# Optimization experiments

Measured on AMD Instinct MI355X. Metric: run time of the kernel, lower is better.

## Reference

```python
import jax, jax.numpy as jnp
import numpy as np

L = 16384          # leaves of complete binary tree
D = 256            # word_dim == tree_input_dim == output_dim
V = 50257          # num_words
NL = 5             # num_labels


def setup_inputs() -> dict:
    key = jax.random.key(0)
    ks = jax.random.split(key, 8)
    s = 0.05
    return {
        "tokens": jax.random.randint(ks[0], (L,), 0, V),
        "emb": jax.random.normal(ks[1], (V, D), jnp.float32) * s,      # word_embedding.weight
        "Wx": jax.random.normal(ks[2], (D, 5 * D), jnp.float32) * s,   # input->gates (leaf only)
        "Ul": jax.random.normal(ks[3], (D, 5 * D), jnp.float32) * s,   # left-child h -> gates
        "Ur": jax.random.normal(ks[4], (D, 5 * D), jnp.float32) * s,   # right-child h -> gates
        "b": jnp.zeros((5 * D,), jnp.float32),
        "Wp": jax.random.normal(ks[5], (D, NL), jnp.float32) * s,      # pred_layer
        "bp": jnp.zeros((NL,), jnp.float32),
    }


def _cell(pre, c_l, c_r):
    # Binary TreeLSTM cell: gates [i, f_l, f_r, o, u]
    i, fl, fr, o, u = jnp.split(pre, 5, axis=-1)
    c = jax.nn.sigmoid(i) * jnp.tanh(u) + jax.nn.sigmoid(fl) * c_l + jax.nn.sigmoid(fr) * c_r
    h = jax.nn.sigmoid(o) * jnp.tanh(c)
    return h, c


def reference(tokens, emb, Wx, Ul, Ur, b, Wp, bp):
    # dropout layers are identity at inference (no-op here)
    x = emb[tokens]                                  # [L, D] seq_output == word embeddings (leaf_rnn=False)
    # leaf nodes: l/r child states are zeros, inputs = seq_out[idx]
    h, c = _cell(x @ Wx + b, 0.0, 0.0)               # [L, D]
    hs = [h]
    # internal nodes level by level (complete binary tree): inputs=None -> no Wx term
    while h.shape[0] > 1:
        hl, hr = h[0::2], h[1::2]
        cl, cr = c[0::2], c[1::2]
        h, c = _cell(hl @ Ul + hr @ Ur + b, cl, cr)
        hs.append(h)
    hidden = jnp.concatenate(hs, axis=0)             # [2L-1, D] all node hidden states
    return hidden @ Wp + bp                          # single_h_pred logits [2L-1, NL]
```

## Files before the change

### kernel.cpp

```cpp
#include <hip/hip_runtime.h>
#include <hip/hip_bf16.h>
#include <math.h>
#include <stdint.h>


typedef __attribute__((ext_vector_type(8))) short     bf16x8;
typedef __attribute__((ext_vector_type(4))) float     f32x4;
typedef __attribute__((ext_vector_type(8))) unsigned short u16x8;

#define NGATE 5

__device__ __forceinline__ uint16_t f2bf(float f) {
    uint32_t u = __builtin_bit_cast(uint32_t, f);
    u = (u + 0x7fffu + ((u >> 16) & 1u)) >> 16;
    return (uint16_t)u;
}
__device__ __forceinline__ float bf2f(uint16_t h) {
    uint32_t u = ((uint32_t)h) << 16;
    return __builtin_bit_cast(float, u);
}
__device__ __forceinline__ float sigf(float x) { return 1.0f / (1.0f + __expf(-x)); }
__device__ __forceinline__ float tanhfast(float x) {
    float e = __expf(2.0f * x);
    return (e - 1.0f) / (e + 1.0f);
}

__device__ __forceinline__ void gld_lds16(const void* g, void* l) {
    __builtin_amdgcn_global_load_lds(
        (const __attribute__((address_space(1))) void*)g,
        (__attribute__((address_space(3))) void*)l,
        16, 0, 0);
}

__global__ __launch_bounds__(256) void pack_w_kernel(
    const float* __restrict__ W0, const float* __restrict__ W1, int KT,
    uint16_t* __restrict__ dhi, uint16_t* __restrict__ dlo)
{
    int gid = blockIdx.x * 256 + threadIdx.x;
    int total = 80 * KT * 64;
    if (gid >= total) return;
    int lane = gid & 63;
    int n  = ((gid >> 6) / KT) * 16 + (lane & 15);
    int kt = (gid >> 6) % KT;
    int k0 = kt * 32 + (lane >> 4) * 8;
    u16x8 vh, vl;
    #pragma unroll
    for (int j = 0; j < 8; ++j) {
        int k = k0 + j;
        const float* src = (k < 256) ? (W0 + (size_t)k * 1280)
                                     : (W1 + (size_t)(k - 256) * 1280);
        float v = src[n];
        uint16_t h = f2bf(v);
        vh[j] = h;
        vl[j] = f2bf(v - bf2f(h));
    }
    *(u16x8*)(dhi + (size_t)gid * 8) = vh;
    *(u16x8*)(dlo + (size_t)gid * 8) = vl;
}

template<int BM, int KT, int JT, bool LVL0>
__global__ __launch_bounds__(256) void lvl_gemm(
    const uint16_t* __restrict__ Ahi, const uint16_t* __restrict__ Alo,
    const int* __restrict__ tokens, const float* __restrict__ emb,
    const uint16_t* __restrict__ Bhi, const uint16_t* __restrict__ Blo,
    const float* __restrict__ b,
    const float* __restrict__ c_prev,
    uint16_t* __restrict__ h_hi_out, uint16_t* __restrict__ h_lo_out,
    float* __restrict__ c_out, int n)
{
    constexpr int K   = KT * 32;
    constexpr int MT  = BM / 64;
    constexpr int ACH = BM / 16;
    constexpr int NC  = NGATE * JT * 2;

    __shared__ __align__(16) uint16_t lA0[2][BM * 32];
    __shared__ __align__(16) uint16_t lA1[2][BM * 32];
    __shared__ __align__(16) uint16_t lB0[NC * 512];
    __shared__ __align__(16) uint16_t lB1[NC * 512];

    const int tid  = threadIdx.x;
    const int wave = tid >> 6;
    const int lane = tid & 63;
    const int quad = lane >> 4;
    const int l15  = lane & 15;
    const int r0   = blockIdx.x * BM;
    const int jn   = blockIdx.y;

    f32x4 acc[MT][JT][NGATE] = {};

    const int row0 = tid >> 1;
    const int kh   = tid & 1;
    const float* esrc = nullptr;
    if constexpr (LVL0) {
        int tok = tokens[r0 + row0];
        esrc = emb + (size_t)tok * 256 + kh * 16;
    }

    auto stageB = [&](uint16_t* dB, int kt) {
        for (int c = wave; c < NC; c += 4) {
            int hl = c & 1, gj = c >> 1;
            const uint16_t* src = hl ? Blo : Bhi;
            int nt = (gj / JT) * 16 + jn * JT + (gj % JT);
            gld_lds16(src + ((size_t)(nt * KT + kt) * 64 + lane) * 8,
                      dB + c * 512);
        }
    };
    auto stageA = [&](uint16_t* dA0, uint16_t* dA1, int kt) {
        for (int c = wave; c < 2 * ACH; c += 4) {
            int mat = (c >= ACH) ? 1 : 0;
            int ci  = mat ? (c - ACH) : c;
            const uint16_t* src = mat ? Alo : Ahi;
            uint16_t* dst = (mat ? dA1 : dA0) + ci * 512;
            int row = r0 + ci * 16 + l15;
            row = min(row, n - 1);
            gld_lds16(src + (size_t)row * K + kt * 32 + quad * 8, dst);
        }
    };
    auto stage0 = [&](uint16_t* dA0, uint16_t* dA1, uint16_t* dB, int kt) {
        stageB(dB, kt);
        const float* s = esrc + kt * 32;
        float v[16];
        #pragma unroll
        for (int q = 0; q < 4; ++q) {
            float4 f = *(const float4*)(s + 4 * q);
            v[4*q+0] = f.x; v[4*q+1] = f.y; v[4*q+2] = f.z; v[4*q+3] = f.w;
        }
        u16x8 h0, h1, l0, l1;
        #pragma unroll
        for (int j = 0; j < 8; ++j) {
            uint16_t h = f2bf(v[j]);     h0[j] = h; l0[j] = f2bf(v[j]     - bf2f(h));
            uint16_t g2 = f2bf(v[j+8]);  h1[j] = g2; l1[j] = f2bf(v[j+8] - bf2f(g2));
        }
        int o = (row0 >> 4) * 512 + kh * 256 + (row0 & 15) * 8;
        *(u16x8*)(dA0 + o)       = h0;
        *(u16x8*)(dA0 + o + 128) = h1;
        *(u16x8*)(dA1 + o)       = l0;
        *(u16x8*)(dA1 + o + 128) = l1;
    };
    auto compute = [&](const uint16_t* A0, const uint16_t* A1, const uint16_t* Bx) {
        bf16x8 ah[MT], al[MT];
        #pragma unroll
        for (int mt = 0; mt < MT; ++mt) {
            int ci = wave * MT + mt;
            ah[mt] = *(const bf16x8*)(A0 + ci * 512 + lane * 8);
            al[mt] = *(const bf16x8*)(A1 + ci * 512 + lane * 8);
        }
        #pragma unroll
        for (int g = 0; g < NGATE; ++g) {
            #pragma unroll
            for (int js = 0; js < JT; ++js) {
                const uint16_t* bp = Bx + (g * JT + js) * 1024;
                bf16x8 bh = *(const bf16x8*)(bp + lane * 8);
                bf16x8 bl = *(const bf16x8*)(bp + 512 + lane * 8);
                #pragma unroll
                for (int mt = 0; mt < MT; ++mt) {
                    acc[mt][js][g] = __builtin_amdgcn_mfma_f32_16x16x32_bf16(ah[mt], bh, acc[mt][js][g], 0, 0, 0);
                    acc[mt][js][g] = __builtin_amdgcn_mfma_f32_16x16x32_bf16(al[mt], bh, acc[mt][js][g], 0, 0, 0);
                    acc[mt][js][g] = __builtin_amdgcn_mfma_f32_16x16x32_bf16(ah[mt], bl, acc[mt][js][g], 0, 0, 0);
                }
            }
        }
    };

    if constexpr (LVL0) stage0(lA0[0], lA0[1], lB0, 0);
    else { stageA(lA0[0], lA0[1], 0); stageB(lB0, 0); }
    __syncthreads();

    for (int kt = 0; kt < KT; kt += 2) {
        if constexpr (LVL0) stage0(lA1[0], lA1[1], lB1, kt + 1);
        else { stageA(lA1[0], lA1[1], kt + 1); stageB(lB1, kt + 1); }
        compute(lA0[0], lA0[1], lB0);
        __syncthreads();

        if (kt + 2 < KT) {
            if constexpr (LVL0) stage0(lA0[0], lA0[1], lB0, kt + 2);
            else { stageA(lA0[0], lA0[1], kt + 2); stageB(lB0, kt + 2); }
        }
        compute(lA1[0], lA1[1], lB1);
        __syncthreads();
    }

    const int d0 = (jn * JT) * 16 + l15;
    float bg[JT][NGATE];
    #pragma unroll
    for (int js = 0; js < JT; ++js)
        #pragma unroll
        for (int g = 0; g < NGATE; ++g) bg[js][g] = b[g * 256 + d0 + js * 16];

    #pragma unroll
    for (int mt = 0; mt < MT; ++mt) {
        int rb = r0 + wave * (MT * 16) + mt * 16 + quad * 4;
        #pragma unroll
        for (int v = 0; v < 4; ++v) {
            int row = rb + v;
            if (row < n) {
                #pragma unroll
                for (int js = 0; js < JT; ++js) {
                    int d = d0 + js * 16;
                    float gi = acc[mt][js][0][v] + bg[js][0];
                    float fl = acc[mt][js][1][v] + bg[js][1];
                    float fr = acc[mt][js][2][v] + bg[js][2];
                    float go = acc[mt][js][3][v] + bg[js][3];
                    float gu = acc[mt][js][4][v] + bg[js][4];
                    float cc;
                    if constexpr (LVL0) {
                        cc = sigf(gi) * tanhfast(gu);
                        (void)fl; (void)fr;
                    } else {
                        float cl = c_prev[(size_t)(2 * row) * 256 + d];
                        float cr = c_prev[(size_t)(2 * row + 1) * 256 + d];
                        cc = sigf(gi) * tanhfast(gu) + sigf(fl) * cl + sigf(fr) * cr;
                    }
                    float hh = sigf(go) * tanhfast(cc);
                    uint16_t hb = f2bf(hh);
                    h_hi_out[(size_t)row * 256 + d] = hb;
                    h_lo_out[(size_t)row * 256 + d] = f2bf(hh - bf2f(hb));
                    c_out[(size_t)row * 256 + d] = cc;
                }
            }
        }
    }
}

__global__ __launch_bounds__(256) void proj_kernel(
    const uint16_t* __restrict__ h_hi, const uint16_t* __restrict__ h_lo,
    const float* __restrict__ Wp, const float* __restrict__ bp,
    float* __restrict__ out, int n)
{
    const int wave = blockIdx.x * 4 + (threadIdx.x >> 6);
    const int lane = threadIdx.x & 63;
    if (wave >= n) return;

    const uint16_t* hh = h_hi + (size_t)wave * 256;
    const uint16_t* hl = h_lo + (size_t)wave * 256;
    float s[5] = {0.f, 0.f, 0.f, 0.f, 0.f};
    #pragma unroll
    for (int q = 0; q < 4; ++q) {
        int dd = lane + 64 * q;
        float hv = bf2f(hh[dd]) + bf2f(hl[dd]);
        #pragma unroll
        for (int j = 0; j < 5; ++j) s[j] += hv * Wp[dd * 5 + j];
    }
    #pragma unroll
    for (int off = 32; off; off >>= 1)
        #pragma unroll
        for (int j = 0; j < 5; ++j) s[j] += __shfl_down(s[j], off);

    if (lane == 0) {
        #pragma unroll
        for (int j = 0; j < 5; ++j) out[(size_t)wave * 5 + j] = s[j] + bp[j];
    }
}

extern "C" void kernel_launch(void* const* d_in, const int* in_sizes, int n_in,
                              void* d_out, int out_size, void* d_ws, size_t ws_size,
                              hipStream_t stream)
{
    const int*   tokens = (const int*)  d_in[0];
    const float* emb    = (const float*)d_in[1];
    const float* Wx     = (const float*)d_in[2];
    const float* Ul     = (const float*)d_in[3];
    const float* Ur     = (const float*)d_in[4];
    const float* b      = (const float*)d_in[5];
    const float* Wp     = (const float*)d_in[6];
    const float* bp     = (const float*)d_in[7];
    float* out = (float*)d_out;

    uint8_t* w = (uint8_t*)d_ws;
    uint16_t* h_hi = (uint16_t*)w;  w += (size_t)32767 * 256 * 2;
    uint16_t* h_lo = (uint16_t*)w;  w += (size_t)32767 * 256 * 2;
    float*    cA   = (float*)w;     w += (size_t)16384 * 256 * 4;
    float*    cB   = (float*)w;     w += (size_t)8192  * 256 * 4;
    uint16_t* BxH  = (uint16_t*)w;  w += (size_t)80 * 8  * 64 * 8 * 2;
    uint16_t* BxL  = (uint16_t*)w;  w += (size_t)80 * 8  * 64 * 8 * 2;
    uint16_t* BuH  = (uint16_t*)w;  w += (size_t)80 * 16 * 64 * 8 * 2;
    uint16_t* BuL  = (uint16_t*)w;  w += (size_t)80 * 16 * 64 * 8 * 2;

    pack_w_kernel<<<(80 * 8  * 64) / 256, 256, 0, stream>>>(Wx, Wx, 8,  BxH, BxL);
    pack_w_kernel<<<(80 * 16 * 64) / 256, 256, 0, stream>>>(Ul, Ur, 16, BuH, BuL);

    int off[16];
    off[0] = 0;
    for (int t = 0; t < 15; ++t) off[t + 1] = off[t] + (16384 >> t);

    lvl_gemm<128, 8, 2, true><<<dim3(16384 / 128, 8), 256, 0, stream>>>(
        nullptr, nullptr, tokens, emb, BxH, BxL, b, nullptr,
        h_hi, h_lo, cA, 16384);

    for (int t = 1; t <= 14; ++t) {
        int n = 16384 >> t;
        const uint16_t* Ah = h_hi + (size_t)off[t - 1] * 256;
        const uint16_t* Al = h_lo + (size_t)off[t - 1] * 256;
        float* c_in  = (t % 2 == 0) ? cB : cA;
        float* c_out = (t % 2 == 0) ? cA : cB;
        uint16_t* Hh = h_hi + (size_t)off[t] * 256;
        uint16_t* Hl = h_lo + (size_t)off[t] * 256;
        if (n >= 4096) {
            lvl_gemm<128, 16, 2, false><<<dim3(n / 128, 8), 256, 0, stream>>>(
                Ah, Al, nullptr, nullptr, BuH, BuL, b, c_in, Hh, Hl, c_out, n);
        } else if (n >= 2048) {
            lvl_gemm<64, 16, 2, false><<<dim3(n / 64, 8), 256, 0, stream>>>(
                Ah, Al, nullptr, nullptr, BuH, BuL, b, c_in, Hh, Hl, c_out, n);
        } else {
            int gx = (n + 63) / 64; if (gx < 1) gx = 1;
            lvl_gemm<64, 16, 1, false><<<dim3(gx, 16), 256, 0, stream>>>(
                Ah, Al, nullptr, nullptr, BuH, BuL, b, c_in, Hh, Hl, c_out, n);
        }
    }

    int total = off[15];
    proj_kernel<<<(total + 3) / 4, 256, 0, stream>>>(h_hi, h_lo, Wp, bp, out, total);
}
```

Measured before the change: 381.3 us.

## Load A operands directly into registers instead of staging through LDS

The A-matrix tiles (child hidden states, or the gathered embeddings at level 0) are now loaded from global memory straight into per-wave registers in MFMA fragment layout, with register double-buffering, instead of being staged through shared memory. Only the B (weight) tiles still go through double-buffered LDS. This cuts LDS capacity use and LDS write/read traffic for A, which may raise occupancy. In exchange it adds register pressure and per-lane global loads that are less coalesced.

```diff
diff --git a/kernel.cpp b/kernel.cpp
--- a/kernel.cpp
+++ b/kernel.cpp
@@ -70,13 +70,10 @@
 {
     constexpr int K   = KT * 32;
     constexpr int MT  = BM / 64;
-    constexpr int ACH = BM / 16;
     constexpr int NC  = NGATE * JT * 2;
 
-    __shared__ __align__(16) uint16_t lA0[2][BM * 32];
-    __shared__ __align__(16) uint16_t lA1[2][BM * 32];
-    __shared__ __align__(16) uint16_t lB0[NC * 512];
-    __shared__ __align__(16) uint16_t lB1[NC * 512];
+    __shared__ __align__(16) uint16_t sB0[NC * 512];
+    __shared__ __align__(16) uint16_t sB1[NC * 512];
 
     const int tid  = threadIdx.x;
     const int wave = tid >> 6;
@@ -88,15 +85,24 @@
 
     f32x4 acc[MT][JT][NGATE] = {};
 
-    const int row0 = tid >> 1;
-    const int kh   = tid & 1;
-    const float* esrc = nullptr;
-    if constexpr (LVL0) {
-        int tok = tokens[r0 + row0];
-        esrc = emb + (size_t)tok * 256 + kh * 16;
+    const uint16_t* aph[MT];
+    const uint16_t* apl[MT];
+    const float*    ebase[MT];
+    #pragma unroll
+    for (int mt = 0; mt < MT; ++mt) {
+        int row = r0 + (wave * MT + mt) * 16 + l15;
+        row = min(row, n - 1);
+        if constexpr (LVL0) {
+            int tok = tokens[row];
+            ebase[mt] = emb + (size_t)tok * 256 + quad * 8;
+        } else {
+            aph[mt] = Ahi + (size_t)row * K + quad * 8;
+            apl[mt] = Alo + (size_t)row * K + quad * 8;
+        }
     }
 
     auto stageB = [&](uint16_t* dB, int kt) {
+        #pragma unroll
         for (int c = wave; c < NC; c += 4) {
             int hl = c & 1, gj = c >> 1;
             const uint16_t* src = hl ? Blo : Bhi;
@@ -105,46 +111,37 @@
                       dB + c * 512);
         }
     };
-    auto stageA = [&](uint16_t* dA0, uint16_t* dA1, int kt) {
-        for (int c = wave; c < 2 * ACH; c += 4) {
-            int mat = (c >= ACH) ? 1 : 0;
-            int ci  = mat ? (c - ACH) : c;
-            const uint16_t* src = mat ? Alo : Ahi;
-            uint16_t* dst = (mat ? dA1 : dA0) + ci * 512;
-            int row = r0 + ci * 16 + l15;
-            row = min(row, n - 1);
-            gld_lds16(src + (size_t)row * K + kt * 32 + quad * 8, dst);
-        }
-    };
-    auto stage0 = [&](uint16_t* dA0, uint16_t* dA1, uint16_t* dB, int kt) {
-        stageB(dB, kt);
-        const float* s = esrc + kt * 32;
-        float v[16];
-        #pragma unroll
-        for (int q = 0; q < 4; ++q) {
-            float4 f = *(const float4*)(s + 4 * q);
-            v[4*q+0] = f.x; v[4*q+1] = f.y; v[4*q+2] = f.z; v[4*q+3] = f.w;
-        }
-        u16x8 h0, h1, l0, l1;
-        #pragma unroll
-        for (int j = 0; j < 8; ++j) {
-            uint16_t h = f2bf(v[j]);     h0[j] = h; l0[j] = f2bf(v[j]     - bf2f(h));
-            uint16_t g2 = f2bf(v[j+8]);  h1[j] = g2; l1[j] = f2bf(v[j+8] - bf2f(g2));
-        }
-        int o = (row0 >> 4) * 512 + kh * 256 + (row0 & 15) * 8;
-        *(u16x8*)(dA0 + o)       = h0;
-        *(u16x8*)(dA0 + o + 128) = h1;
-        *(u16x8*)(dA1 + o)       = l0;
-        *(u16x8*)(dA1 + o + 128) = l1;
-    };
-    auto compute = [&](const uint16_t* A0, const uint16_t* A1, const uint16_t* Bx) {
-        bf16x8 ah[MT], al[MT];
+    auto loadAn = [&](bf16x8 (&ah)[MT], bf16x8 (&al)[MT], int kt) {
         #pragma unroll
         for (int mt = 0; mt < MT; ++mt) {
-            int ci = wave * MT + mt;
-            ah[mt] = *(const bf16x8*)(A0 + ci * 512 + lane * 8);
-            al[mt] = *(const bf16x8*)(A1 + ci * 512 + lane * 8);
-        }
+            ah[mt] = *(const bf16x8*)(aph[mt] + kt * 32);
+            al[mt] = *(const bf16x8*)(apl[mt] + kt * 32);
+        }
+    };
+    auto loadA0 = [&](float4 (&e)[MT][2], int kt) {
+        #pragma unroll
+        for (int mt = 0; mt < MT; ++mt) {
+            const float4* p = (const float4*)(ebase[mt] + kt * 32);
+            e[mt][0] = p[0];
+            e[mt][1] = p[1];
+        }
+    };
+    auto cvtA0 = [&](const float4 (&e)[MT][2], bf16x8 (&ah)[MT], bf16x8 (&al)[MT]) {
+        #pragma unroll
+        for (int mt = 0; mt < MT; ++mt) {
+            float fv[8];
+            fv[0] = e[mt][0].x; fv[1] = e[mt][0].y; fv[2] = e[mt][0].z; fv[3] = e[mt][0].w;
+            fv[4] = e[mt][1].x; fv[5] = e[mt][1].y; fv[6] = e[mt][1].z; fv[7] = e[mt][1].w;
+            #pragma unroll
+            for (int j = 0; j < 8; ++j) {
+                uint16_t h = f2bf(fv[j]);
+                ah[mt][j] = (short)h;
+                al[mt][j] = (short)f2bf(fv[j] - bf2f(h));
+            }
+        }
+    };
+    auto mfma_all = [&](const bf16x8 (&ah)[MT], const bf16x8 (&al)[MT],
+                        const uint16_t* Bx) {
         #pragma unroll
         for (int g = 0; g < NGATE; ++g) {
             #pragma unroll
@@ -162,22 +159,42 @@
         }
     };
 
-    if constexpr (LVL0) stage0(lA0[0], lA0[1], lB0, 0);
-    else { stageA(lA0[0], lA0[1], 0); stageB(lB0, 0); }
-    __syncthreads();
-
-    for (int kt = 0; kt < KT; kt += 2) {
-        if constexpr (LVL0) stage0(lA1[0], lA1[1], lB1, kt + 1);
-        else { stageA(lA1[0], lA1[1], kt + 1); stageB(lB1, kt + 1); }
-        compute(lA0[0], lA0[1], lB0);
+    if constexpr (LVL0) {
+        float4 eA[MT][2], eB[MT][2];
+        loadA0(eA, 0);
+        stageB(sB0, 0);
         __syncthreads();
-
-        if (kt + 2 < KT) {
-            if constexpr (LVL0) stage0(lA0[0], lA0[1], lB0, kt + 2);
-            else { stageA(lA0[0], lA0[1], kt + 2); stageB(lB0, kt + 2); }
-        }
-        compute(lA1[0], lA1[1], lB1);
+        for (int kt = 0; kt < KT; kt += 2) {
+            loadA0(eB, kt + 1);
+            stageB(sB1, kt + 1);
+            {
+                bf16x8 ah[MT], al[MT];
+                cvtA0(eA, ah, al);
+                mfma_all(ah, al, sB0);
+            }
+            __syncthreads();
+            if (kt + 2 < KT) { loadA0(eA, kt + 2); stageB(sB0, kt + 2); }
+            {
+                bf16x8 ah[MT], al[MT];
+                cvtA0(eB, ah, al);
+                mfma_all(ah, al, sB1);
+            }
+            __syncthreads();
+        }
+    } else {
+        bf16x8 hA[MT], lA[MT], hB[MT], lB[MT];
+        loadAn(hA, lA, 0);
+        stageB(sB0, 0);
         __syncthreads();
+        for (int kt = 0; kt < KT; kt += 2) {
+            loadAn(hB, lB, kt + 1);
+            stageB(sB1, kt + 1);
+            mfma_all(hA, lA, sB0);
+            __syncthreads();
+            if (kt + 2 < KT) { loadAn(hA, lA, kt + 2); stageB(sB0, kt + 2); }
+            mfma_all(hB, lB, sB1);
+            __syncthreads();
+        }
     }
 
     const int d0 = (jn * JT) * 16 + l15;
```

Result: faster. 340.3 us (-10.8%).
